# Optimization experiments

Hardware: AMD Instinct MI355X
Metric: run time of the kernel (lower is better)

## Reference

```python
import jax, jax.numpy as jnp
import numpy as np
import math

B, S, D, H = 4, 2048, 1024, 16
HD = D // H  # head dim = 64

def setup_inputs() -> dict:
    key = jax.random.key(0)
    ks = jax.random.split(key, 8)
    scale = 1.0 / math.sqrt(D)
    return {
        "hidden_states": jax.random.normal(ks[0], (B, S, D), jnp.float32),
        "attention_mask": jnp.zeros((B, 1, 1, S), jnp.float32),
        "Wq": jax.random.normal(ks[1], (D, D), jnp.float32) * scale,
        "bq": jnp.zeros((D,), jnp.float32),
        "Wk": jax.random.normal(ks[2], (D, D), jnp.float32) * scale,
        "bk": jnp.zeros((D,), jnp.float32),
        "Wv": jax.random.normal(ks[3], (D, D), jnp.float32) * scale,
        "bv": jnp.zeros((D,), jnp.float32),
    }

def _split_heads(x):
    # [B,S,D] -> [B,H,S,HD]
    return x.reshape(B, S, H, HD).transpose(0, 2, 1, 3)

def reference(hidden_states, attention_mask, Wq, bq, Wk, bk, Wv, bv):
    q = _split_heads(hidden_states @ Wq + bq)
    k = _split_heads(hidden_states @ Wk + bk)
    v = _split_heads(hidden_states @ Wv + bv)
    scores = jnp.einsum("bhqd,bhkd->bhqk", q, k) / math.sqrt(HD)
    scores = scores + attention_mask
    probs = jax.nn.softmax(scores, axis=-1)
    ctx = jnp.einsum("bhqk,bhkd->bhqd", probs, v)
    # [B,H,S,HD] -> [B,S,D]
    return ctx.transpose(0, 2, 1, 3).reshape(B, S, D)
```

## Files before the change

kernel.cpp:

```cpp
#include <hip/hip_runtime.h>
#include <hip/hip_bf16.h>
#include <stdint.h>

#define Bc 4
#define Sc 2048
#define Dc 1024
#define Hc 16
#define HDc 64
#define LOG2E 1.44269504088896f

typedef __attribute__((ext_vector_type(8))) __bf16 bf16x8;
typedef __attribute__((ext_vector_type(4))) __bf16 bf16x4;
typedef __attribute__((ext_vector_type(4))) float f32x4;
typedef __attribute__((ext_vector_type(16))) float f32x16;
typedef __attribute__((ext_vector_type(2))) int i32x2_t;

__device__ __forceinline__ f32x4 mfma16(bf16x8 a, bf16x8 b, f32x4 c) {
  return __builtin_amdgcn_mfma_f32_16x16x32_bf16(a, b, c, 0, 0, 0);
}
__device__ __forceinline__ f32x16 mfma32(bf16x8 a, bf16x8 b, f32x16 c) {
  return __builtin_amdgcn_mfma_f32_32x32x16_bf16(a, b, c, 0, 0, 0);
}
__device__ __forceinline__ uint32_t cvtpk_bf16(float lo, float hi) {
  uint32_t r;
  asm("v_cvt_pk_bf16_f32 %0, %1, %2" : "=v"(r) : "v"(lo), "v"(hi));
  return r;
}
__device__ __forceinline__ void gload_lds16(const void* g, void* l) {
  __builtin_amdgcn_global_load_lds(
      (const __attribute__((address_space(1))) void*)g,
      (__attribute__((address_space(3))) void*)l, 16, 0, 0);
}
__device__ __forceinline__ void gload_lds4(const void* g, void* l) {
  __builtin_amdgcn_global_load_lds(
      (const __attribute__((address_space(1))) void*)g,
      (__attribute__((address_space(3))) void*)l, 4, 0, 0);
}

__global__ __launch_bounds__(256) void maskscale_kernel(const float* __restrict__ m,
                                                        float* __restrict__ mkx) {
  const int i = blockIdx.x * 256 + threadIdx.x;
  mkx[i] = m[i] * LOG2E;
}

__global__ __launch_bounds__(256) void hs2bf_kernel(const float* __restrict__ hs,
                                                    __bf16* __restrict__ Ah) {
  const size_t i = ((size_t)blockIdx.x * 256 + threadIdx.x) * 8;
  float4 f0 = *(const float4*)(hs + i);
  float4 f1 = *(const float4*)(hs + i + 4);
  bf16x8 o;
  o[0] = (__bf16)f0.x; o[1] = (__bf16)f0.y; o[2] = (__bf16)f0.z; o[3] = (__bf16)f0.w;
  o[4] = (__bf16)f1.x; o[5] = (__bf16)f1.y; o[6] = (__bf16)f1.z; o[7] = (__bf16)f1.w;
  *(bf16x8*)(Ah + i) = o;
}

__global__ __launch_bounds__(256) void wtrans_kernel(
    const float* __restrict__ Wq, const float* __restrict__ Wk,
    const float* __restrict__ Wv, __bf16* __restrict__ Wt) {
  const float* W = (blockIdx.z == 0) ? Wq : (blockIdx.z == 1 ? Wk : Wv);
  __bf16* out = Wt + (size_t)blockIdx.z * Dc * Dc;
  const int n0 = blockIdx.x * 64, k0 = blockIdx.y * 64;
  __shared__ float tile[64][65];
  const int tid = threadIdx.x;
  const int r = tid >> 2, cs = (tid & 3) * 16;
  const float* src = W + (size_t)(k0 + r) * Dc + n0 + cs;
  float4 f0 = *(const float4*)(src + 0);
  float4 f1 = *(const float4*)(src + 4);
  float4 f2 = *(const float4*)(src + 8);
  float4 f3 = *(const float4*)(src + 12);
#pragma unroll
  for (int j = 0; j < 4; ++j) {
    tile[r][cs + j] = ((const float*)&f0)[j];
    tile[r][cs + 4 + j] = ((const float*)&f1)[j];
    tile[r][cs + 8 + j] = ((const float*)&f2)[j];
    tile[r][cs + 12 + j] = ((const float*)&f3)[j];
  }
  __syncthreads();
  bf16x8 o0, o1;
#pragma unroll
  for (int j = 0; j < 8; ++j) {
    o0[j] = (__bf16)tile[cs + j][r];
    o1[j] = (__bf16)tile[cs + 8 + j][r];
  }
  __bf16* dst = out + (size_t)(n0 + r) * Dc + k0 + cs;
  *(bf16x8*)(dst) = o0;
  *(bf16x8*)(dst + 8) = o1;
}

__global__ __launch_bounds__(512) void qkv_gemm_kernel(
    const __bf16* __restrict__ A, const __bf16* __restrict__ Wt,
    const float* __restrict__ bq, const float* __restrict__ bk,
    const float* __restrict__ bv,
    __bf16* __restrict__ Qo, __bf16* __restrict__ Kf, __bf16* __restrict__ Vf) {
  const int wg = (blockIdx.x & 7) * 96 + (blockIdx.x >> 3);
  const int nn = wg >> 6;
  const int mm = wg & 63;
  const int m0 = mm * 128;
  const int n0 = nn * 256;
  const int w = n0 >> 10;
  const int nbase = n0 & 1023;

  const float* bias = (w == 0) ? bq : (w == 1 ? bk : bv);

  __shared__ __attribute__((aligned(16))) __bf16 Asm[3][4096];
  __shared__ __attribute__((aligned(16))) __bf16 Bsm[3][8192];

  const int tid = threadIdx.x, lane = tid & 63, wid = tid >> 6;
  const int wr = wid >> 2, wc = wid & 3;
  const int lg = lane >> 4, li = lane & 15;

  f32x4 acc[4][4] = {};

  auto stage = [&](int buf, int kt) {
    const int k0 = kt * 32;
    {
      const int row = tid >> 2;
      const int sc = (tid & 3) ^ (row & 3);
      gload_lds16(A + (size_t)(m0 + row) * Dc + k0 + sc * 8,
                  &Asm[buf][wid * 512]);
    }
#pragma unroll
    for (int p = 0; p < 2; ++p) {
      const int row = p * 128 + (tid >> 2);
      const int sc = (tid & 3) ^ (row & 3);
      gload_lds16(Wt + (size_t)(n0 + row) * Dc + k0 + sc * 8,
                  &Bsm[buf][p * 4096 + wid * 512]);
    }
  };

  const int aoff = (wr * 64 + li) * 32 + ((lg ^ (li & 3)) * 8);
  const int boff = (wc * 64 + li) * 32 + ((lg ^ (li & 3)) * 8);

  stage(0, 0);
  stage(1, 1);
  for (int ks = 0; ks < 32; ++ks) {
    asm volatile("s_waitcnt vmcnt(3)" ::: "memory");
    __builtin_amdgcn_sched_barrier(0);
    __builtin_amdgcn_s_barrier();
    __builtin_amdgcn_sched_barrier(0);
    {
      const int tn = (ks + 2 < 32) ? ks + 2 : 31;
      stage((ks + 2) % 3, tn);
    }
    const __bf16* Ab = &Asm[ks % 3][0] + aoff;
    const __bf16* Bb = &Bsm[ks % 3][0] + boff;
    bf16x8 af[4], bfr[4];
#pragma unroll
    for (int i = 0; i < 4; ++i) af[i] = *(const bf16x8*)(Ab + i * 512);
#pragma unroll
    for (int j = 0; j < 4; ++j) bfr[j] = *(const bf16x8*)(Bb + j * 512);
    __builtin_amdgcn_s_setprio(1);
#pragma unroll
    for (int i = 0; i < 4; ++i)
#pragma unroll
      for (int j = 0; j < 4; ++j)
        acc[i][j] = mfma16(af[i], bfr[j], acc[i][j]);
    __builtin_amdgcn_s_setprio(0);
  }

  if (w == 0) {
    const float scl = 0.125f * LOG2E;
#pragma unroll
    for (int i = 0; i < 4; ++i) {
#pragma unroll
      for (int j = 0; j < 4; ++j) {
        const int n = nbase + wc * 64 + j * 16 + li;
        const float bb = bias[n];
        const int h = n >> 6, hd = n & 63;
#pragma unroll
        for (int r = 0; r < 4; ++r) {
          const int m = m0 + wr * 64 + i * 16 + lg * 4 + r;
          const int b = m >> 11, s = m & 2047;
          Qo[(((size_t)b * Hc + h) * Sc + s) * HDc + hd] =
              (__bf16)((acc[i][j][r] + bb) * scl);
        }
      }
    }
  } else if (w == 1) {
#pragma unroll
    for (int j = 0; j < 4; ++j) {
      const int n = nbase + wc * 64 + j * 16 + li;
      const float bb = bias[n];
      const int h = n >> 6, hd = n & 63;
      const int c = hd >> 4, shi = (hd >> 3) & 1, j8 = hd & 7;
#pragma unroll
      for (int i = 0; i < 4; ++i) {
#pragma unroll
        for (int r = 0; r < 4; ++r) {
          const int m = m0 + wr * 64 + i * 16 + lg * 4 + r;
          const int b = m >> 11, s = m & 2047;
          const int bh = b * Hc + h;
          const int t = s >> 6, kt = s & 63;
          const int slot = (kt >> 5) * 256 + c * 64 + shi * 32 + (kt & 31);
          Kf[((size_t)(bh * 32 + t)) * 4096 + slot * 8 + j8] =
              (__bf16)(acc[i][j][r] + bb);
        }
      }
    }
  } else {
#pragma unroll
    for (int i = 0; i < 4; ++i) {
      const int mbase = m0 + wr * 64 + i * 16 + lg * 4;
      const int b = mbase >> 11, sk = mbase & 2047;
      const int t = sk >> 6, kt = sk & 63;
      const int kc = kt >> 4, shi = (kt >> 3) & 1, j0 = kt & 7;
#pragma unroll
      for (int j = 0; j < 4; ++j) {
        const int n = nbase + wc * 64 + j * 16 + li;
        const float bb = bias[n];
        const int h = n >> 6, hd = n & 63;
        const int nb = hd >> 5, sqr = hd & 31;
        const int bh = b * Hc + h;
        const int slot = kc * 128 + nb * 64 + shi * 32 + sqr;
        bf16x4 o;
#pragma unroll
        for (int r = 0; r < 4; ++r) o[r] = (__bf16)(acc[i][j][r] + bb);
        *(bf16x4*)&Vf[((size_t)(bh * 32 + t)) * 4096 + slot * 8 + j0] = o;
      }
    }
  }
}

__global__ __launch_bounds__(512) void attn_kernel(
    const __bf16* __restrict__ Q, const __bf16* __restrict__ Kf,
    const __bf16* __restrict__ Vf, const float* __restrict__ mkx,
    float* __restrict__ out) {
  const int idx = blockIdx.x;
  const int bh = (idx & 7) | (((idx >> 3) & 7) << 3);
  const int qt = idx >> 6;
  const int b = bh >> 4, h = bh & 15;
  const __bf16* qb = Q + (size_t)bh * Sc * HDc;
  const __bf16* kfb = Kf + (size_t)bh * 32 * 4096;
  const __bf16* vfb = Vf + (size_t)bh * 32 * 4096;
  const float* mb = mkx + (size_t)b * Sc;

  const int tid = threadIdx.x, lane = tid & 63, wid = tid >> 6;
  const int hi = lane >> 5, qr = lane & 31;

  __shared__ __attribute__((aligned(16))) __bf16 Ksm[3][4096];
  __shared__ __attribute__((aligned(16))) __bf16 Vsm[3][4096];
  __shared__ __attribute__((aligned(16))) float Msm[3][64];

  const int q0 = qt * 256 + wid * 32;

  bf16x8 qf[4];
#pragma unroll
  for (int c = 0; c < 4; ++c)
    qf[c] = *(const bf16x8*)(qb + (size_t)(q0 + qr) * HDc + c * 16 + hi * 8);

  bf16x8 onesv;
#pragma unroll
  for (int j = 0; j < 8; ++j) onesv[j] = (__bf16)1.0f;

  f32x16 oacc[2] = {};
  f32x16 lacc = {};
  f32x16 sA[2], sB[2];

  auto stage = [&](int buf, int t) {
    const size_t tb = (size_t)t * 4096;
    gload_lds16(kfb + tb + (size_t)tid * 8, &Ksm[buf][wid * 512]);
    gload_lds16(vfb + tb + (size_t)tid * 8, &Vsm[buf][wid * 512]);
    gload_lds4(mb + t * 64 + lane, &Msm[buf][0]);
  };

  auto qk = [&](int buf, f32x16 (&s)[2]) {
    const __bf16* Kb = &Ksm[buf][0] + lane * 8;
    const float* Mb = &Msm[buf][0];
#pragma unroll
    for (int kb2 = 0; kb2 < 2; ++kb2) {
#pragma unroll
      for (int g = 0; g < 4; ++g) {
        const float4 m4 = *(const float4*)&Mb[kb2 * 32 + g * 8 + hi * 4];
#pragma unroll
        for (int e = 0; e < 4; ++e) s[kb2][g * 4 + e] = ((const float*)&m4)[e];
      }
    }
    __builtin_amdgcn_s_setprio(1);
#pragma unroll
    for (int kb2 = 0; kb2 < 2; ++kb2) {
#pragma unroll
      for (int c = 0; c < 4; ++c) {
        const bf16x8 kf = *(const bf16x8*)(Kb + (kb2 * 4 + c) * 512);
        s[kb2] = mfma32(kf, qf[c], s[kb2]);
      }
    }
    __builtin_amdgcn_s_setprio(0);
  };

  auto softpv = [&](int buf, f32x16 (&s)[2]) {
    const __bf16* Vb = &Vsm[buf][0] + lane * 8;
    bf16x8 pa[4];
#pragma unroll
    for (int kb2 = 0; kb2 < 2; ++kb2) {
      uint32_t wv[8];
#pragma unroll
      for (int j = 0; j < 8; ++j)
        wv[j] = cvtpk_bf16(__builtin_amdgcn_exp2f(s[kb2][2 * j]),
                           __builtin_amdgcn_exp2f(s[kb2][2 * j + 1]));
#pragma unroll
      for (int cc = 0; cc < 2; ++cc) {
        i32x2_t s02 = __builtin_amdgcn_permlane32_swap(
            (int)wv[cc * 4 + 0], (int)wv[cc * 4 + 2], false, false);
        i32x2_t s13 = __builtin_amdgcn_permlane32_swap(
            (int)wv[cc * 4 + 1], (int)wv[cc * 4 + 3], false, false);
        union { uint32_t u[4]; bf16x8 v; } af;
        af.u[0] = (uint32_t)s02[0];
        af.u[1] = (uint32_t)s13[0];
        af.u[2] = (uint32_t)s02[1];
        af.u[3] = (uint32_t)s13[1];
        pa[kb2 * 2 + cc] = af.v;
      }
    }
    __builtin_amdgcn_s_setprio(1);
#pragma unroll
    for (int kc = 0; kc < 4; ++kc) {
      lacc = mfma32(pa[kc], onesv, lacc);
#pragma unroll
      for (int nb = 0; nb < 2; ++nb) {
        const bf16x8 vf = *(const bf16x8*)(Vb + (kc * 2 + nb) * 512);
        oacc[nb] = mfma32(pa[kc], vf, oacc[nb]);
      }
    }
    __builtin_amdgcn_s_setprio(0);
  };

  const int NT = Sc / 64;

  stage(0, 0);
  stage(1, 1);
  __builtin_amdgcn_sched_barrier(0);
  asm volatile("s_waitcnt vmcnt(3)" ::: "memory");
  __builtin_amdgcn_s_barrier();
  __builtin_amdgcn_sched_barrier(0);
  qk(0, sA);

#define ITER(T, PB, QB, SB, CUR, NXT)                                   \
  {                                                                     \
    const int t_ = (T);                                                 \
    const int tn_ = (t_ + 2 < NT) ? t_ + 2 : NT - 1;                    \
    asm volatile("s_waitcnt vmcnt(0)" ::: "memory");                    \
    __builtin_amdgcn_sched_barrier(0);                                  \
    __builtin_amdgcn_s_barrier();                                       \
    __builtin_amdgcn_sched_barrier(0);                                  \
    stage(SB, tn_);                                                     \
    qk(QB, NXT);                                                        \
    softpv(PB, CUR);                                                    \
  }

  for (int t6 = 0; t6 < 30; t6 += 6) {
    ITER(t6 + 0, 0, 1, 2, sA, sB);
    ITER(t6 + 1, 1, 2, 0, sB, sA);
    ITER(t6 + 2, 2, 0, 1, sA, sB);
    ITER(t6 + 3, 0, 1, 2, sB, sA);
    ITER(t6 + 4, 1, 2, 0, sA, sB);
    ITER(t6 + 5, 2, 0, 1, sB, sA);
  }
  ITER(30, 0, 1, 2, sA, sB);
  ITER(31, 1, 2, 0, sB, sA);
#undef ITER

  float inv[16];
#pragma unroll
  for (int r = 0; r < 16; ++r) inv[r] = __builtin_amdgcn_rcpf(lacc[r]);
#pragma unroll
  for (int nb = 0; nb < 2; ++nb) {
#pragma unroll
    for (int r = 0; r < 16; ++r) {
      const int row = (r & 3) + 8 * (r >> 2) + 4 * hi;
      const int qg = q0 + row;
      out[((size_t)b * Sc + qg) * Dc + h * HDc + nb * 32 + qr] =
          oacc[nb][r] * inv[r];
    }
  }
}

extern "C" void kernel_launch(void* const* d_in, const int* in_sizes, int n_in,
                              void* d_out, int out_size, void* d_ws,
                              size_t ws_size, hipStream_t stream) {
  const float* hs = (const float*)d_in[0];
  const float* mask = (const float*)d_in[1];
  const float* Wq = (const float*)d_in[2];
  const float* bq = (const float*)d_in[3];
  const float* Wk = (const float*)d_in[4];
  const float* bk = (const float*)d_in[5];
  const float* Wv = (const float*)d_in[6];
  const float* bv = (const float*)d_in[7];
  float* out = (float*)d_out;

  char* ws = (char*)d_ws;
  const size_t qkv_bytes = (size_t)Bc * Hc * Sc * HDc * 2;
  __bf16* Wt = (__bf16*)ws;
  __bf16* Ah = (__bf16*)(ws + 6291456);
  __bf16* Q = (__bf16*)(ws + 6291456 + qkv_bytes);
  __bf16* Kf = (__bf16*)(ws + 6291456 + 2 * qkv_bytes);
  __bf16* Vf = (__bf16*)(ws + 6291456 + 3 * qkv_bytes);
  float* mkx = (float*)(ws + 6291456 + 4 * qkv_bytes);

  maskscale_kernel<<<32, 256, 0, stream>>>(mask, mkx);
  hs2bf_kernel<<<4096, 256, 0, stream>>>(hs, Ah);
  wtrans_kernel<<<dim3(16, 16, 3), 256, 0, stream>>>(Wq, Wk, Wv, Wt);
  qkv_gemm_kernel<<<768, 512, 0, stream>>>(Ah, Wt, bq, bk, bv, Q, Kf, Vf);
  attn_kernel<<<512, 512, 0, stream>>>(Q, Kf, Vf, mkx, out);
}
```

Baseline: 174.6 us.

## Process two 32-row query tiles per wave in attention with 256-thread blocks

The attention kernel now runs 4 waves per block, and each wave handles two 32-row query groups (q0 and q0+128), so every K/V fragment read from LDS feeds twice as many MFMAs. Staging loads twice as much per thread to fill the same 64-key tile. The QK-of-next/softmax-PV-of-current software pipeline is replaced by a single fused body per tile with a looser vmcnt wait. The change also remaps block index to bh and roughly doubles accumulator register pressure per wave, which risks lower occupancy and losing cross-tile overlap.

```diff
diff --git a/kernel.cpp b/kernel.cpp
--- a/kernel.cpp
+++ b/kernel.cpp
@@ -221,12 +221,12 @@
   }
 }
 
-__global__ __launch_bounds__(512) void attn_kernel(
+__global__ __launch_bounds__(256) void attn_kernel(
     const __bf16* __restrict__ Q, const __bf16* __restrict__ Kf,
     const __bf16* __restrict__ Vf, const float* __restrict__ mkx,
     float* __restrict__ out) {
   const int idx = blockIdx.x;
-  const int bh = (idx & 7) | (((idx >> 3) & 7) << 3);
+  const int bh = (idx & 7) * 8 + ((idx >> 3) & 7);
   const int qt = idx >> 6;
   const int b = bh >> 4, h = bh & 15;
   const __bf16* qb = Q + (size_t)bh * Sc * HDc;
@@ -243,36 +243,47 @@
 
   const int q0 = qt * 256 + wid * 32;
 
-  bf16x8 qf[4];
-#pragma unroll
-  for (int c = 0; c < 4; ++c)
-    qf[c] = *(const bf16x8*)(qb + (size_t)(q0 + qr) * HDc + c * 16 + hi * 8);
+  bf16x8 qfA[4], qfB[4];
+#pragma unroll
+  for (int c = 0; c < 4; ++c) {
+    qfA[c] = *(const bf16x8*)(qb + (size_t)(q0 + qr) * HDc + c * 16 + hi * 8);
+    qfB[c] = *(const bf16x8*)(qb + (size_t)(q0 + 128 + qr) * HDc + c * 16 + hi * 8);
+  }
 
   bf16x8 onesv;
 #pragma unroll
   for (int j = 0; j < 8; ++j) onesv[j] = (__bf16)1.0f;
 
-  f32x16 oacc[2] = {};
-  f32x16 lacc = {};
-  f32x16 sA[2], sB[2];
+  f32x16 oaccA[2] = {}, oaccB[2] = {};
+  f32x16 laccA = {}, laccB = {};
 
   auto stage = [&](int buf, int t) {
     const size_t tb = (size_t)t * 4096;
-    gload_lds16(kfb + tb + (size_t)tid * 8, &Ksm[buf][wid * 512]);
-    gload_lds16(vfb + tb + (size_t)tid * 8, &Vsm[buf][wid * 512]);
+#pragma unroll
+    for (int p = 0; p < 2; ++p) {
+      gload_lds16(kfb + tb + p * 2048 + (size_t)tid * 8,
+                  &Ksm[buf][p * 2048 + wid * 512]);
+      gload_lds16(vfb + tb + p * 2048 + (size_t)tid * 8,
+                  &Vsm[buf][p * 2048 + wid * 512]);
+    }
     gload_lds4(mb + t * 64 + lane, &Msm[buf][0]);
   };
 
-  auto qk = [&](int buf, f32x16 (&s)[2]) {
+  auto body = [&](int buf) {
     const __bf16* Kb = &Ksm[buf][0] + lane * 8;
+    const __bf16* Vb = &Vsm[buf][0] + lane * 8;
     const float* Mb = &Msm[buf][0];
+    f32x16 sa[2], sb2[2];
 #pragma unroll
     for (int kb2 = 0; kb2 < 2; ++kb2) {
 #pragma unroll
       for (int g = 0; g < 4; ++g) {
         const float4 m4 = *(const float4*)&Mb[kb2 * 32 + g * 8 + hi * 4];
 #pragma unroll
-        for (int e = 0; e < 4; ++e) s[kb2][g * 4 + e] = ((const float*)&m4)[e];
+        for (int e = 0; e < 4; ++e) {
+          sa[kb2][g * 4 + e] = ((const float*)&m4)[e];
+          sb2[kb2][g * 4 + e] = ((const float*)&m4)[e];
+        }
       }
     }
     __builtin_amdgcn_s_setprio(1);
@@ -281,95 +292,96 @@
 #pragma unroll
       for (int c = 0; c < 4; ++c) {
         const bf16x8 kf = *(const bf16x8*)(Kb + (kb2 * 4 + c) * 512);
-        s[kb2] = mfma32(kf, qf[c], s[kb2]);
+        sa[kb2] = mfma32(kf, qfA[c], sa[kb2]);
+        sb2[kb2] = mfma32(kf, qfB[c], sb2[kb2]);
+      }
+    }
+    __builtin_amdgcn_s_setprio(0);
+
+    bf16x8 paA[4], paB[4];
+#pragma unroll
+    for (int set = 0; set < 2; ++set) {
+      f32x16* s = (set == 0) ? sa : sb2;
+      bf16x8* pa = (set == 0) ? paA : paB;
+#pragma unroll
+      for (int kb2 = 0; kb2 < 2; ++kb2) {
+        uint32_t wv[8];
+#pragma unroll
+        for (int j = 0; j < 8; ++j)
+          wv[j] = cvtpk_bf16(__builtin_amdgcn_exp2f(s[kb2][2 * j]),
+                             __builtin_amdgcn_exp2f(s[kb2][2 * j + 1]));
+#pragma unroll
+        for (int cc = 0; cc < 2; ++cc) {
+          i32x2_t s02 = __builtin_amdgcn_permlane32_swap(
+              (int)wv[cc * 4 + 0], (int)wv[cc * 4 + 2], false, false);
+          i32x2_t s13 = __builtin_amdgcn_permlane32_swap(
+              (int)wv[cc * 4 + 1], (int)wv[cc * 4 + 3], false, false);
+          union { uint32_t u[4]; bf16x8 v; } af;
+          af.u[0] = (uint32_t)s02[0];
+          af.u[1] = (uint32_t)s13[0];
+          af.u[2] = (uint32_t)s02[1];
+          af.u[3] = (uint32_t)s13[1];
+          pa[kb2 * 2 + cc] = af.v;
+        }
+      }
+    }
+
+    __builtin_amdgcn_s_setprio(1);
+#pragma unroll
+    for (int kc = 0; kc < 4; ++kc) {
+      laccA = mfma32(paA[kc], onesv, laccA);
+      laccB = mfma32(paB[kc], onesv, laccB);
+#pragma unroll
+      for (int nb = 0; nb < 2; ++nb) {
+        const bf16x8 vf = *(const bf16x8*)(Vb + (kc * 2 + nb) * 512);
+        oaccA[nb] = mfma32(paA[kc], vf, oaccA[nb]);
+        oaccB[nb] = mfma32(paB[kc], vf, oaccB[nb]);
       }
     }
     __builtin_amdgcn_s_setprio(0);
   };
 
-  auto softpv = [&](int buf, f32x16 (&s)[2]) {
-    const __bf16* Vb = &Vsm[buf][0] + lane * 8;
-    bf16x8 pa[4];
-#pragma unroll
-    for (int kb2 = 0; kb2 < 2; ++kb2) {
-      uint32_t wv[8];
-#pragma unroll
-      for (int j = 0; j < 8; ++j)
-        wv[j] = cvtpk_bf16(__builtin_amdgcn_exp2f(s[kb2][2 * j]),
-                           __builtin_amdgcn_exp2f(s[kb2][2 * j + 1]));
-#pragma unroll
-      for (int cc = 0; cc < 2; ++cc) {
-        i32x2_t s02 = __builtin_amdgcn_permlane32_swap(
-            (int)wv[cc * 4 + 0], (int)wv[cc * 4 + 2], false, false);
-        i32x2_t s13 = __builtin_amdgcn_permlane32_swap(
-            (int)wv[cc * 4 + 1], (int)wv[cc * 4 + 3], false, false);
-        union { uint32_t u[4]; bf16x8 v; } af;
-        af.u[0] = (uint32_t)s02[0];
-        af.u[1] = (uint32_t)s13[0];
-        af.u[2] = (uint32_t)s02[1];
-        af.u[3] = (uint32_t)s13[1];
-        pa[kb2 * 2 + cc] = af.v;
-      }
-    }
-    __builtin_amdgcn_s_setprio(1);
-#pragma unroll
-    for (int kc = 0; kc < 4; ++kc) {
-      lacc = mfma32(pa[kc], onesv, lacc);
-#pragma unroll
-      for (int nb = 0; nb < 2; ++nb) {
-        const bf16x8 vf = *(const bf16x8*)(Vb + (kc * 2 + nb) * 512);
-        oacc[nb] = mfma32(pa[kc], vf, oacc[nb]);
-      }
-    }
-    __builtin_amdgcn_s_setprio(0);
-  };
-
   const int NT = Sc / 64;
 
   stage(0, 0);
   stage(1, 1);
-  __builtin_amdgcn_sched_barrier(0);
-  asm volatile("s_waitcnt vmcnt(3)" ::: "memory");
-  __builtin_amdgcn_s_barrier();
-  __builtin_amdgcn_sched_barrier(0);
-  qk(0, sA);
-
-#define ITER(T, PB, QB, SB, CUR, NXT)                                   \
+
+#define ITER(T, PB, SB)                                                 \
   {                                                                     \
     const int t_ = (T);                                                 \
     const int tn_ = (t_ + 2 < NT) ? t_ + 2 : NT - 1;                    \
-    asm volatile("s_waitcnt vmcnt(0)" ::: "memory");                    \
+    asm volatile("s_waitcnt vmcnt(5)" ::: "memory");                    \
     __builtin_amdgcn_sched_barrier(0);                                  \
     __builtin_amdgcn_s_barrier();                                       \
     __builtin_amdgcn_sched_barrier(0);                                  \
     stage(SB, tn_);                                                     \
-    qk(QB, NXT);                                                        \
-    softpv(PB, CUR);                                                    \
-  }
-
-  for (int t6 = 0; t6 < 30; t6 += 6) {
-    ITER(t6 + 0, 0, 1, 2, sA, sB);
-    ITER(t6 + 1, 1, 2, 0, sB, sA);
-    ITER(t6 + 2, 2, 0, 1, sA, sB);
-    ITER(t6 + 3, 0, 1, 2, sB, sA);
-    ITER(t6 + 4, 1, 2, 0, sA, sB);
-    ITER(t6 + 5, 2, 0, 1, sB, sA);
-  }
-  ITER(30, 0, 1, 2, sA, sB);
-  ITER(31, 1, 2, 0, sB, sA);
+    body(PB);                                                           \
+  }
+
+  for (int t3 = 0; t3 < 30; t3 += 3) {
+    ITER(t3 + 0, 0, 2);
+    ITER(t3 + 1, 1, 0);
+    ITER(t3 + 2, 2, 1);
+  }
+  ITER(30, 0, 2);
+  ITER(31, 1, 0);
 #undef ITER
 
-  float inv[16];
-#pragma unroll
-  for (int r = 0; r < 16; ++r) inv[r] = __builtin_amdgcn_rcpf(lacc[r]);
+  float invA[16], invB[16];
+#pragma unroll
+  for (int r = 0; r < 16; ++r) {
+    invA[r] = __builtin_amdgcn_rcpf(laccA[r]);
+    invB[r] = __builtin_amdgcn_rcpf(laccB[r]);
+  }
 #pragma unroll
   for (int nb = 0; nb < 2; ++nb) {
 #pragma unroll
     for (int r = 0; r < 16; ++r) {
       const int row = (r & 3) + 8 * (r >> 2) + 4 * hi;
-      const int qg = q0 + row;
-      out[((size_t)b * Sc + qg) * Dc + h * HDc + nb * 32 + qr] =
-          oacc[nb][r] * inv[r];
+      out[((size_t)b * Sc + q0 + row) * Dc + h * HDc + nb * 32 + qr] =
+          oaccA[nb][r] * invA[r];
+      out[((size_t)b * Sc + q0 + 128 + row) * Dc + h * HDc + nb * 32 + qr] =
+          oaccB[nb][r] * invB[r];
     }
   }
 }
@@ -400,5 +412,5 @@
   hs2bf_kernel<<<4096, 256, 0, stream>>>(hs, Ah);
   wtrans_kernel<<<dim3(16, 16, 3), 256, 0, stream>>>(Wq, Wk, Wv, Wt);
   qkv_gemm_kernel<<<768, 512, 0, stream>>>(Ah, Wt, bq, bk, bv, Q, Kf, Vf);
-  attn_kernel<<<512, 512, 0, stream>>>(Q, Kf, Vf, mkx, out);
-}
+  attn_kernel<<<512, 256, 0, stream>>>(Q, Kf, Vf, mkx, out);
+}
```

Measured after the change: 199.3 us. +14.2%, slower.
